# Performance work log

Hardware: AMD Instinct MI355X
Metric: run time of the kernel (lower is better)

The kernel has to match this reference:

```python
import jax, jax.numpy as jnp
import numpy as np

N = 100000      # nodes
E = 3200000     # edges (before self-loops)
IN = 1          # input feature dim
H1, C = 4, 8    # layer1: 4 heads x 8 channels; layer2: 1 head x 8 channels
NEG_SLOPE = 0.2


def setup_inputs() -> dict:
    key = jax.random.key(0)
    ks = jax.random.split(key, 10)
    x = jax.random.normal(ks[0], (N, IN), jnp.float32)
    edge_index = jax.random.randint(ks[1], (2, E), 0, N, dtype=jnp.int32)
    # layer 1 params (GATConv(1, 8, heads=4))
    W1 = jax.random.normal(ks[2], (IN, H1 * C), jnp.float32) * 0.5
    a_src1 = jax.random.normal(ks[3], (H1, C), jnp.float32) * 0.5
    a_dst1 = jax.random.normal(ks[4], (H1, C), jnp.float32) * 0.5
    b1 = jnp.zeros((H1 * C,), jnp.float32)
    # layer 2 params (GATConv(32, 8, heads=1))
    W2 = jax.random.normal(ks[5], (H1 * C, C), jnp.float32) * 0.2
    a_src2 = jax.random.normal(ks[6], (1, C), jnp.float32) * 0.5
    a_dst2 = jax.random.normal(ks[7], (1, C), jnp.float32) * 0.5
    b2 = jnp.zeros((C,), jnp.float32)
    return {"x": x, "edge_index": edge_index, "W1": W1, "a_src1": a_src1,
            "a_dst1": a_dst1, "b1": b1, "W2": W2, "a_src2": a_src2,
            "a_dst2": a_dst2, "b2": b2}


def _gat_layer(x, src, dst, W, a_s, a_d, b, heads, ch):
    # Linear transform per head: [N, heads, ch]
    h = (x @ W).reshape(-1, heads, ch)
    # per-node attention logits
    al_s = jnp.einsum('nhc,hc->nh', h, a_s)  # [N, H]
    al_d = jnp.einsum('nhc,hc->nh', h, a_d)  # [N, H]
    # per-edge logits (message src -> dst)
    e = jax.nn.leaky_relu(al_s[src] + al_d[dst], NEG_SLOPE)  # [E', H]
    # segment softmax over incoming edges of each dst node
    m = jax.ops.segment_max(e, dst, num_segments=N)          # [N, H]
    e = jnp.exp(e - m[dst])
    s = jax.ops.segment_sum(e, dst, num_segments=N)          # [N, H]
    alpha = e / s[dst]                                       # [E', H]
    # weighted scatter-add aggregation
    out = jax.ops.segment_sum(h[src] * alpha[:, :, None], dst, num_segments=N)
    return out.reshape(N, heads * ch) + b


def reference(x, edge_index, W1, a_src1, a_dst1, b1, W2, a_src2, a_dst2, b2):
    loops = jnp.arange(N, dtype=edge_index.dtype)
    src = jnp.concatenate([edge_index[0], loops])  # add self-loops (PyG default)
    dst = jnp.concatenate([edge_index[1], loops])
    h = _gat_layer(x, src, dst, W1, a_src1, a_dst1, b1, H1, C)
    h = jax.nn.relu(h)
    out = _gat_layer(h, src, dst, W2, a_src2, a_dst2, b2, 1, C)
    return out
```

## Files before the change

kernel.cpp:

```cpp
#include <hip/hip_runtime.h>
#include <hip/hip_bf16.h>

#define NEG_SLOPE 0.2f
#define CAPS 8192
#define CAPG 8192
#define CAPA 81920


__global__ void init_cc(int* __restrict__ curA, int* __restrict__ curB,
                        const float* __restrict__ W1,
                        const float* __restrict__ as1,
                        const float* __restrict__ ad1,
                        float* __restrict__ consts) {
    int t = threadIdx.x;
    if (t < 8) {
        int h = t & 3;
        const float* a = (t < 4) ? as1 : ad1;
        float s = 0.f;
        #pragma unroll
        for (int c = 0; c < 8; ++c)
            s += W1[h * 8 + c] * a[h * 8 + c];
        consts[t] = s;
    }
    if (t < 64) curA[t] = t * CAPA;
    curB[t] = t << 13;
}

__global__ void scatterA(const int* __restrict__ ei, int* __restrict__ curA,
                         unsigned int* __restrict__ bufA, int E) {
    __shared__ int cnt[64];
    __shared__ int basel[64];
    int t = threadIdx.x;
    int chunk = (E + gridDim.x - 1) / gridDim.x;
    int lo = blockIdx.x * chunk;
    int hi = min(E, lo + chunk);
    const int* dei = ei + E;
    if (t < 64) cnt[t] = 0;
    __syncthreads();
    bool vec = ((E & 3) == 0);
    int lo4 = (lo + 3) & ~3;
    int end4 = hi & ~3;
    if (vec && end4 > lo4) {
        for (int e = lo + t; e < lo4; e += 1024) atomicAdd(&cnt[dei[e] >> 11], 1);
        const int4* dei4 = (const int4*)dei;
        for (int v = (lo4 >> 2) + t; v < (end4 >> 2); v += 1024) {
            int4 d = dei4[v];
            atomicAdd(&cnt[d.x >> 11], 1); atomicAdd(&cnt[d.y >> 11], 1);
            atomicAdd(&cnt[d.z >> 11], 1); atomicAdd(&cnt[d.w >> 11], 1);
        }
        for (int e = end4 + t; e < hi; e += 1024) atomicAdd(&cnt[dei[e] >> 11], 1);
    } else {
        for (int e = lo + t; e < hi; e += 1024) atomicAdd(&cnt[dei[e] >> 11], 1);
    }
    __syncthreads();
    if (t < 64) {
        int c = cnt[t];
        basel[t] = c ? (atomicAdd(&curA[t], c) - t * CAPA) : 0;
        cnt[t] = 0;
    }
    __syncthreads();
    if (vec && end4 > lo4) {
        for (int e = lo + t; e < lo4; e += 1024) {
            int s = ei[e], d = dei[e]; int sp = d >> 11;
            int off = basel[sp] + atomicAdd(&cnt[sp], 1);
            if (off < CAPA) bufA[sp * CAPA + off] = (unsigned)s | ((unsigned)(d & 2047) << 17);
        }
        const int4* sei4 = (const int4*)ei;
        const int4* dei4 = (const int4*)dei;
        for (int v = (lo4 >> 2) + t; v < (end4 >> 2); v += 1024) {
            int4 sv = sei4[v]; int4 dv = dei4[v];
            int s0 = dv.x >> 11, s1 = dv.y >> 11, s2 = dv.z >> 11, s3 = dv.w >> 11;
            int o0 = basel[s0] + atomicAdd(&cnt[s0], 1);
            if (o0 < CAPA) bufA[s0 * CAPA + o0] = (unsigned)sv.x | ((unsigned)(dv.x & 2047) << 17);
            int o1 = basel[s1] + atomicAdd(&cnt[s1], 1);
            if (o1 < CAPA) bufA[s1 * CAPA + o1] = (unsigned)sv.y | ((unsigned)(dv.y & 2047) << 17);
            int o2 = basel[s2] + atomicAdd(&cnt[s2], 1);
            if (o2 < CAPA) bufA[s2 * CAPA + o2] = (unsigned)sv.z | ((unsigned)(dv.z & 2047) << 17);
            int o3 = basel[s3] + atomicAdd(&cnt[s3], 1);
            if (o3 < CAPA) bufA[s3 * CAPA + o3] = (unsigned)sv.w | ((unsigned)(dv.w & 2047) << 17);
        }
        for (int e = end4 + t; e < hi; e += 1024) {
            int s = ei[e], d = dei[e]; int sp = d >> 11;
            int off = basel[sp] + atomicAdd(&cnt[sp], 1);
            if (off < CAPA) bufA[sp * CAPA + off] = (unsigned)s | ((unsigned)(d & 2047) << 17);
        }
    } else {
        for (int e = lo + t; e < hi; e += 1024) {
            int s = ei[e], d = dei[e]; int sp = d >> 11;
            int off = basel[sp] + atomicAdd(&cnt[sp], 1);
            if (off < CAPA) bufA[sp * CAPA + off] = (unsigned)s | ((unsigned)(d & 2047) << 17);
        }
    }
}

__global__ void scatterB(const int* __restrict__ curA, int* __restrict__ curB,
                         const unsigned int* __restrict__ bufA,
                         unsigned int* __restrict__ pairs) {
    __shared__ int cnt[16];
    __shared__ int basel[16];
    int t = threadIdx.x;
    int sp = blockIdx.x >> 3;
    int part = blockIdx.x & 7;
    int base = sp * CAPA;
    int fill = min(curA[sp] - base, CAPA);
    if (fill <= 0) return;
    int lo = (fill * part) >> 3;
    int hi = (fill * (part + 1)) >> 3;
    for (int c0 = lo; c0 < hi; c0 += 8192) {
        int cend = min(hi, c0 + 8192);
        if (t < 16) cnt[t] = 0;
        __syncthreads();
        for (int i = c0 + t; i < cend; i += 1024)
            atomicAdd(&cnt[(bufA[base + i] >> 24) & 15], 1);
        __syncthreads();
        if (t < 16) {
            int c = cnt[t];
            int bkg = (sp << 4) + t;
            basel[t] = c ? (atomicAdd(&curB[bkg], c) - (bkg << 13)) : 0;
            cnt[t] = 0;
        }
        __syncthreads();
        for (int i = c0 + t; i < cend; i += 1024) {
            unsigned p = bufA[base + i];
            int b16 = (p >> 24) & 15;
            int off = basel[b16] + atomicAdd(&cnt[b16], 1);
            if (off < CAPG) pairs[(((sp << 4) + b16) << 13) + off] = p & 0x00FFFFFFu;
        }
        __syncthreads();
    }
}

__global__ __launch_bounds__(512, 8)
void l1_comb(const float* __restrict__ x,
             const int* __restrict__ curB,
             const unsigned int* __restrict__ pairs,
             unsigned int* __restrict__ gsorted, int* __restrict__ bmeta,
             const float* __restrict__ consts,
             const float* __restrict__ W1, const float* __restrict__ b1,
             const float* __restrict__ W2,
             const float* __restrict__ as2, const float* __restrict__ ad2,
             float* __restrict__ h2, float* __restrict__ als2,
             float* __restrict__ ald2, int N) {
    __shared__ unsigned sbuf[CAPS];
    __shared__ int hcnt[128], offs[128], hcur[128];
    __shared__ float xl[128];
    int t = threadIdx.x;
    int bk = blockIdx.x;
    int node0 = bk << 7;
    int nw = min(128, N - node0);
    if (t < 128) xl[t] = (t < nw) ? x[node0 + t] : 0.f;
    float S[4], D[4];
    #pragma unroll
    for (int h = 0; h < 4; ++h) { S[h] = consts[h]; D[h] = consts[4 + h]; }
    int base = bk << 13;
    int clen = min(curB[bk] - base, CAPG);
    int clen6 = min(clen, 6144);
    int g = t >> 2, jj = t & 3;
    unsigned pr[12];
    const uint4* pairs4 = (const uint4*)(pairs + base);
    #pragma unroll
    for (int k = 0; k < 3; ++k) {
        int w4 = t + (k << 9);
        int wi = w4 << 2;
        if (wi + 3 < clen6) {
            uint4 v = pairs4[w4];
            pr[4 * k]     = v.x; pr[4 * k + 1] = v.y;
            pr[4 * k + 2] = v.z; pr[4 * k + 3] = v.w;
        } else {
            #pragma unroll
            for (int m = 0; m < 4; ++m)
                pr[4 * k + m] = (wi + m < clen6) ? pairs[base + wi + m] : 0xFFFFFFFFu;
        }
    }
    if (t < 128) hcnt[t] = 0;
    __syncthreads();
    #pragma unroll
    for (int k = 0; k < 12; ++k)
        if (pr[k] != 0xFFFFFFFFu) atomicAdd(&hcnt[pr[k] >> 17], 1);
    for (int idx = 6144 + t; idx < clen; idx += 512)
        atomicAdd(&hcnt[pairs[base + idx] >> 17], 1);
    __syncthreads();
    if (t < 64) {
        int h0 = hcnt[2 * t], h1 = hcnt[2 * t + 1];
        int s = h0 + h1, sc_ = s;
        #pragma unroll
        for (int o = 1; o < 64; o <<= 1) {
            int u = __shfl_up(sc_, o);
            if (t >= o) sc_ += u;
        }
        int excl = sc_ - s;
        offs[2 * t] = excl;          hcur[2 * t] = excl;
        offs[2 * t + 1] = excl + h0; hcur[2 * t + 1] = excl + h0;
    }
    __syncthreads();
    #pragma unroll
    for (int k = 0; k < 12; ++k)
        if (pr[k] != 0xFFFFFFFFu) {
            int loc = atomicAdd(&hcur[pr[k] >> 17], 1);
            sbuf[loc] = pr[k];
        }
    for (int idx = 6144 + t; idx < clen; idx += 512) {
        unsigned p = pairs[base + idx];
        int loc = atomicAdd(&hcur[p >> 17], 1);
        sbuf[loc] = p;
    }
    __syncthreads();
    {
        int clen4 = clen & ~3;
        for (int i = t << 2; i < clen4; i += 2048) {
            uint4 v = *(const uint4*)&sbuf[i];
            *(uint4*)&gsorted[base + i] = v;
        }
        for (int i = clen4 + t; i < clen; i += 512) gsorted[base + i] = sbuf[i];
    }
    if (t < 128) bmeta[(bk << 7) + t] = offs[t] | (hcnt[t] << 14);
    float xd = xl[g];
    float sacc[4] = {0.f, 0.f, 0.f, 0.f};
    float tacc[4] = {0.f, 0.f, 0.f, 0.f};
    int st = offs[g], en = st + hcnt[g];
    int i = st + jj;
    while (i + 28 < en) {
        unsigned p0 = sbuf[i],      p1 = sbuf[i + 4],  p2 = sbuf[i + 8],
                 p3 = sbuf[i + 12], p4 = sbuf[i + 16], p5 = sbuf[i + 20],
                 p6 = sbuf[i + 24], p7 = sbuf[i + 28];
        float x0 = x[p0 & 131071u], x1 = x[p1 & 131071u];
        float x2 = x[p2 & 131071u], x3 = x[p3 & 131071u];
        float x4 = x[p4 & 131071u], x5 = x[p5 & 131071u];
        float x6 = x[p6 & 131071u], x7 = x[p7 & 131071u];
        float xs_[8] = {x0, x1, x2, x3, x4, x5, x6, x7};
        #pragma unroll
        for (int q = 0; q < 8; ++q) {
            float xs = xs_[q];
            #pragma unroll
            for (int h = 0; h < 4; ++h) {
                float v = xs * S[h] + xd * D[h];
                v = (v > 0.f) ? v : NEG_SLOPE * v;
                float w = __expf(v);
                sacc[h] += w;
                tacc[h] = fmaf(w, xs, tacc[h]);
            }
        }
        i += 32;
    }
    for (; i < en; i += 4) {
        float xs = x[sbuf[i] & 131071u];
        #pragma unroll
        for (int h = 0; h < 4; ++h) {
            float v = xs * S[h] + xd * D[h];
            v = (v > 0.f) ? v : NEG_SLOPE * v;
            float w = __expf(v);
            sacc[h] += w;
            tacc[h] = fmaf(w, xs, tacc[h]);
        }
    }
    #pragma unroll
    for (int h = 0; h < 4; ++h) {
        sacc[h] += __shfl_xor(sacc[h], 1); sacc[h] += __shfl_xor(sacc[h], 2);
        tacc[h] += __shfl_xor(tacc[h], 1); tacc[h] += __shfl_xor(tacc[h], 2);
    }
    if (jj == 0 && g < nw) {
        int n = node0 + g;
        float xn = xd;
        float o[8];
        #pragma unroll
        for (int c = 0; c < 8; ++c) o[c] = 0.f;
        #pragma unroll
        for (int h = 0; h < 4; ++h) {
            float v = xn * (S[h] + D[h]);
            v = (v > 0.f) ? v : NEG_SLOPE * v;
            float ww = __expf(v);
            float s1 = ww + sacc[h];
            float t1 = ww * xn + tacc[h];
            float tt = t1 / s1;
            #pragma unroll
            for (int c = 0; c < 8; ++c) {
                float rr = fmaxf(tt * W1[h * 8 + c] + b1[h * 8 + c], 0.f);
                #pragma unroll
                for (int c2 = 0; c2 < 8; ++c2) o[c2] += rr * W2[(h * 8 + c) * 8 + c2];
            }
        }
        float as = 0.f, ad = 0.f;
        #pragma unroll
        for (int c = 0; c < 8; ++c) { as += o[c] * as2[c]; ad += o[c] * ad2[c]; }
        float4* hv = (float4*)&h2[(size_t)n * 8];
        hv[0] = make_float4(o[0], o[1], o[2], o[3]);
        hv[1] = make_float4(o[4], o[5], o[6], o[7]);
        als2[n] = as;
        ald2[n] = ad;
    }
}

__global__ __launch_bounds__(512, 8)
void l2_comb(const int* __restrict__ curB,
             const unsigned int* __restrict__ gsorted,
             const int* __restrict__ bmeta,
             const float* __restrict__ als2, const float* __restrict__ ald2,
             const float* __restrict__ h2, const float* __restrict__ b2,
             float* __restrict__ out, int N) {
    __shared__ unsigned runl[CAPS];
    __shared__ float adl[128];
    int t = threadIdx.x;
    int bk = blockIdx.x;
    int node0 = bk << 7;
    int nw = min(128, N - node0);
    if (t < 128) adl[t] = (t < nw) ? ald2[node0 + t] : 0.f;
    int base = bk << 13;
    int clen = min(curB[bk] - base, CAPG);
    {
        int clen4 = clen & ~3;
        const uint4* g4 = (const uint4*)(gsorted + base);
        for (int i = t << 2; i < clen4; i += 2048) {
            uint4 v = g4[i >> 2];
            *(uint4*)&runl[i] = v;
        }
        for (int i = clen4 + t; i < clen; i += 512) runl[i] = gsorted[base + i];
    }
    __syncthreads();
    int g = t >> 2, j = t & 3;
    int jh = j & 1;
    int jp = j >> 1;
    if (g >= nw) return;
    int pk = bmeta[(bk << 7) + g];
    int st = pk & 16383, cgn = pk >> 14;
    const unsigned* run = runl + st;
    float adv = adl[g];
    int co = jh << 2;
    float4 acc = make_float4(0.f, 0.f, 0.f, 0.f);
    float sw = 0.f;
    int k = 0;
    while (2 * k + 8 <= cgn) {
        unsigned q0 = run[2 * k + jp];
        unsigned q1 = run[2 * k + 2 + jp];
        unsigned q2 = run[2 * k + 4 + jp];
        unsigned q3 = run[2 * k + 6 + jp];
        size_t r0 = (size_t)(q0 & 131071u) * 8 + co;
        size_t r1 = (size_t)(q1 & 131071u) * 8 + co;
        size_t r2 = (size_t)(q2 & 131071u) * 8 + co;
        size_t r3 = (size_t)(q3 & 131071u) * 8 + co;
        float4 h0 = *(const float4*)&h2[r0];
        float4 h1 = *(const float4*)&h2[r1];
        float4 h2v = *(const float4*)&h2[r2];
        float4 h3 = *(const float4*)&h2[r3];
        float a0 = als2[q0 & 131071u], a1 = als2[q1 & 131071u];
        float a2 = als2[q2 & 131071u], a3 = als2[q3 & 131071u];
        float aa[4] = {a0, a1, a2, a3};
        float4 hh[4] = {h0, h1, h2v, h3};
        #pragma unroll
        for (int q = 0; q < 4; ++q) {
            float v = aa[q] + adv;
            v = (v > 0.f) ? v : NEG_SLOPE * v;
            float w = __expf(v);
            sw += w;
            acc.x = fmaf(w, hh[q].x, acc.x);
            acc.y = fmaf(w, hh[q].y, acc.y);
            acc.z = fmaf(w, hh[q].z, acc.z);
            acc.w = fmaf(w, hh[q].w, acc.w);
        }
        k += 4;
    }
    for (; 2 * k + jp < cgn; ++k) {
        unsigned q = run[2 * k + jp];
        size_t r = (size_t)(q & 131071u) * 8 + co;
        float4 hq = *(const float4*)&h2[r];
        float a = als2[q & 131071u];
        float v = a + adv;
        v = (v > 0.f) ? v : NEG_SLOPE * v;
        float w = __expf(v);
        sw += w;
        acc.x = fmaf(w, hq.x, acc.x);
        acc.y = fmaf(w, hq.y, acc.y);
        acc.z = fmaf(w, hq.z, acc.z);
        acc.w = fmaf(w, hq.w, acc.w);
    }
    acc.x += __shfl_xor(acc.x, 2); acc.y += __shfl_xor(acc.y, 2);
    acc.z += __shfl_xor(acc.z, 2); acc.w += __shfl_xor(acc.w, 2);
    sw += __shfl_xor(sw, 2);
    int n = node0 + g;
    float v = als2[n] + adv;
    v = (v > 0.f) ? v : NEG_SLOPE * v;
    float ww = __expf(v);
    float4 hs = *(const float4*)&h2[(size_t)n * 8 + co];
    float inv = 1.f / (sw + ww);
    if (jp == 0) {
        float4 bb = *(const float4*)&b2[co];
        *(float4*)&out[(size_t)n * 8 + co] = make_float4(
            (acc.x + ww * hs.x) * inv + bb.x,
            (acc.y + ww * hs.y) * inv + bb.y,
            (acc.z + ww * hs.z) * inv + bb.z,
            (acc.w + ww * hs.w) * inv + bb.w);
    }
}


__global__ void prep_consts(const float* __restrict__ W1,
                            const float* __restrict__ as1,
                            const float* __restrict__ ad1,
                            float* __restrict__ consts) {
    int t = threadIdx.x;
    if (t >= 8) return;
    int h = t & 3;
    const float* a = (t < 4) ? as1 : ad1;
    float s = 0.f;
    #pragma unroll
    for (int c = 0; c < 8; ++c)
        s += W1[h * 8 + c] * a[h * 8 + c];
    consts[t] = s;
}

__global__ void edge_pass1(const int* __restrict__ ei, const float* __restrict__ x,
                           const float* __restrict__ consts,
                           float* __restrict__ s1, float* __restrict__ t1, int E, int N) {
    int e = blockIdx.x * blockDim.x + threadIdx.x;
    if (e >= E + N) return;
    int src, dst;
    if (e < E) { src = ei[e]; dst = ei[E + e]; }
    else       { src = dst = e - E; }
    float xs = x[src], xd = x[dst];
    #pragma unroll
    for (int h = 0; h < 4; ++h) {
        float v = xs * consts[h] + xd * consts[4 + h];
        v = (v > 0.f) ? v : NEG_SLOPE * v;
        float w = __expf(v);
        atomicAdd(&s1[dst * 4 + h], w);
        atomicAdd(&t1[dst * 4 + h], w * xs);
    }
}

__global__ void node_mid(const float* __restrict__ s1, const float* __restrict__ t1,
                         const float* __restrict__ W1, const float* __restrict__ b1,
                         const float* __restrict__ W2,
                         const float* __restrict__ as2, const float* __restrict__ ad2,
                         float* __restrict__ h2, float* __restrict__ als2,
                         float* __restrict__ ald2, int N) {
    int n = blockIdx.x * blockDim.x + threadIdx.x;
    if (n >= N) return;
    float o[8];
    #pragma unroll
    for (int c = 0; c < 8; ++c) o[c] = 0.f;
    #pragma unroll
    for (int h = 0; h < 4; ++h) {
        float t = t1[n * 4 + h] / s1[n * 4 + h];
        #pragma unroll
        for (int c = 0; c < 8; ++c) {
            float r = fmaxf(t * W1[h * 8 + c] + b1[h * 8 + c], 0.f);
            #pragma unroll
            for (int c2 = 0; c2 < 8; ++c2) o[c2] += r * W2[(h * 8 + c) * 8 + c2];
        }
    }
    float as = 0.f, ad = 0.f;
    #pragma unroll
    for (int c = 0; c < 8; ++c) { h2[n * 8 + c] = o[c]; as += o[c] * as2[c]; ad += o[c] * ad2[c]; }
    als2[n] = as; ald2[n] = ad;
}

__global__ void edge_pass2(const int* __restrict__ ei, const float* __restrict__ als2,
                           const float* __restrict__ ald2, const float* __restrict__ h2,
                           float* __restrict__ s2, float* __restrict__ acc2, int E, int N) {
    int e = blockIdx.x * blockDim.x + threadIdx.x;
    if (e >= E + N) return;
    int src, dst;
    if (e < E) { src = ei[e]; dst = ei[E + e]; }
    else       { src = dst = e - E; }
    float v = als2[src] + ald2[dst];
    v = (v > 0.f) ? v : NEG_SLOPE * v;
    float w = __expf(v);
    atomicAdd(&s2[dst], w);
    const float4* hs = (const float4*)&h2[src * 8];
    float4 a = hs[0], bq = hs[1];
    float* acc = &acc2[dst * 8];
    atomicAdd(&acc[0], w * a.x);  atomicAdd(&acc[1], w * a.y);
    atomicAdd(&acc[2], w * a.z);  atomicAdd(&acc[3], w * a.w);
    atomicAdd(&acc[4], w * bq.x); atomicAdd(&acc[5], w * bq.y);
    atomicAdd(&acc[6], w * bq.z); atomicAdd(&acc[7], w * bq.w);
}

__global__ void node_out(const float* __restrict__ s2, const float* __restrict__ acc2,
                         const float* __restrict__ b2, float* __restrict__ out, int N) {
    int i = blockIdx.x * blockDim.x + threadIdx.x;
    if (i >= N * 8) return;
    out[i] = acc2[i] / s2[i >> 3] + b2[i & 7];
}


extern "C" void kernel_launch(void* const* d_in, const int* in_sizes, int n_in,
                              void* d_out, int out_size, void* d_ws, size_t ws_size,
                              hipStream_t stream) {
    const float* x   = (const float*)d_in[0];
    const int*   ei  = (const int*)d_in[1];
    const float* W1  = (const float*)d_in[2];
    const float* as1 = (const float*)d_in[3];
    const float* ad1 = (const float*)d_in[4];
    const float* b1  = (const float*)d_in[5];
    const float* W2  = (const float*)d_in[6];
    const float* as2 = (const float*)d_in[7];
    const float* ad2 = (const float*)d_in[8];
    const float* b2  = (const float*)d_in[9];
    float* out = (float*)d_out;

    const int N = in_sizes[0];
    const int E = in_sizes[1] / 2;
    const int NBK = (N + 127) >> 7;

    float* ws = (float*)d_ws;
    size_t need = ((size_t)16 + 64 + 1024 + 131072 + 10 * (size_t)N
                   + 2 * (size_t)1024 * CAPG + (size_t)64 * CAPA) * sizeof(float);

    if (N <= 131072 && ws_size >= need) {
        float*    consts  = ws;
        int*      curA    = (int*)(ws + 16);
        int*      curB    = curA + 64;
        int*      bmeta   = curB + 1024;
        float*    als2    = (float*)(bmeta + 131072);
        float*    ald2    = als2 + N;
        float*    h2      = ald2 + N;
        unsigned* pairs   = (unsigned*)(h2 + 8 * (size_t)N);
        unsigned* gsorted = pairs + (size_t)1024 * CAPG;
        unsigned* bufA    = gsorted + (size_t)1024 * CAPG;

        init_cc<<<1, 1024, 0, stream>>>(curA, curB, W1, as1, ad1, consts);
        scatterA<<<256, 1024, 0, stream>>>(ei, curA, bufA, E);
        scatterB<<<512, 1024, 0, stream>>>(curA, curB, bufA, pairs);
        l1_comb<<<NBK, 512, 0, stream>>>(x, curB, pairs, gsorted, bmeta, consts,
                                         W1, b1, W2, as2, ad2, h2, als2, ald2, N);
        l2_comb<<<NBK, 512, 0, stream>>>(curB, gsorted, bmeta, als2, ald2, h2, b2, out, N);
    } else {
        float* consts = ws;
        float* s1   = ws + 16;
        float* t1   = s1 + 4 * (size_t)N;
        float* h2   = t1 + 4 * (size_t)N;
        float* als2 = h2 + 8 * (size_t)N;
        float* ald2 = als2 + (size_t)N;
        float* s2   = ald2 + (size_t)N;
        float* acc2 = s2 + (size_t)N;

        hipMemsetAsync(ws, 0, (16 + 8 * (size_t)N) * sizeof(float), stream);
        hipMemsetAsync(s2, 0, 9 * (size_t)N * sizeof(float), stream);
        prep_consts<<<1, 64, 0, stream>>>(W1, as1, ad1, consts);
        int total = E + N;
        edge_pass1<<<(total + 255) / 256, 256, 0, stream>>>(ei, x, consts, s1, t1, E, N);
        node_mid<<<(N + 255) / 256, 256, 0, stream>>>(s1, t1, W1, b1, W2, as2, ad2, h2, als2, ald2, N);
        edge_pass2<<<(total + 255) / 256, 256, 0, stream>>>(ei, als2, ald2, h2, s2, acc2, E, N);
        node_out<<<(N * 8 + 255) / 256, 256, 0, stream>>>(s2, acc2, b2, out, N);
    }
}
```

Baseline: 179.2 us.

## Use per-block fixed segments in scatterA to drop count pass and global atomics

scatterA now writes each block's edges for a superbucket into a fixed-width private segment, and records the per-block fill in a table. This removes the separate counting pass over the destination indices and the global atomic reservation on curA. scatterB reads its 32 segments using the fill table. The init kernel is replaced by a memset, and the per-head attention constants are recomputed inside l1_comb. The risk is that a segment overflows (fixed cap of 384 entries per block per superbucket) and silently drops edges when the degree distribution is skewed; scatterB also makes a second pass over bufA with per-segment loops.

```diff
diff --git a/kernel.cpp b/kernel.cpp
--- a/kernel.cpp
+++ b/kernel.cpp
@@ -4,35 +4,18 @@
 #define NEG_SLOPE 0.2f
 #define CAPS 8192
 #define CAPG 8192
-#define CAPA 81920
-
-
-__global__ void init_cc(int* __restrict__ curA, int* __restrict__ curB,
-                        const float* __restrict__ W1,
-                        const float* __restrict__ as1,
-                        const float* __restrict__ ad1,
-                        float* __restrict__ consts) {
+#define SEGW 384
+#define CAPA (256 * SEGW)
+
+
+__global__ void scatterA(const int* __restrict__ ei,
+                         unsigned int* __restrict__ bufA,
+                         int* __restrict__ fillT, int E) {
+    __shared__ int cnt[64];
     int t = threadIdx.x;
-    if (t < 8) {
-        int h = t & 3;
-        const float* a = (t < 4) ? as1 : ad1;
-        float s = 0.f;
-        #pragma unroll
-        for (int c = 0; c < 8; ++c)
-            s += W1[h * 8 + c] * a[h * 8 + c];
-        consts[t] = s;
-    }
-    if (t < 64) curA[t] = t * CAPA;
-    curB[t] = t << 13;
-}
-
-__global__ void scatterA(const int* __restrict__ ei, int* __restrict__ curA,
-                         unsigned int* __restrict__ bufA, int E) {
-    __shared__ int cnt[64];
-    __shared__ int basel[64];
-    int t = threadIdx.x;
+    int blk = blockIdx.x;
     int chunk = (E + gridDim.x - 1) / gridDim.x;
-    int lo = blockIdx.x * chunk;
+    int lo = blk * chunk;
     int hi = min(E, lo + chunk);
     const int* dei = ei + E;
     if (t < 64) cnt[t] = 0;
@@ -41,59 +24,42 @@
     int lo4 = (lo + 3) & ~3;
     int end4 = hi & ~3;
     if (vec && end4 > lo4) {
-        for (int e = lo + t; e < lo4; e += 1024) atomicAdd(&cnt[dei[e] >> 11], 1);
-        const int4* dei4 = (const int4*)dei;
-        for (int v = (lo4 >> 2) + t; v < (end4 >> 2); v += 1024) {
-            int4 d = dei4[v];
-            atomicAdd(&cnt[d.x >> 11], 1); atomicAdd(&cnt[d.y >> 11], 1);
-            atomicAdd(&cnt[d.z >> 11], 1); atomicAdd(&cnt[d.w >> 11], 1);
-        }
-        for (int e = end4 + t; e < hi; e += 1024) atomicAdd(&cnt[dei[e] >> 11], 1);
-    } else {
-        for (int e = lo + t; e < hi; e += 1024) atomicAdd(&cnt[dei[e] >> 11], 1);
-    }
-    __syncthreads();
-    if (t < 64) {
-        int c = cnt[t];
-        basel[t] = c ? (atomicAdd(&curA[t], c) - t * CAPA) : 0;
-        cnt[t] = 0;
-    }
-    __syncthreads();
-    if (vec && end4 > lo4) {
         for (int e = lo + t; e < lo4; e += 1024) {
             int s = ei[e], d = dei[e]; int sp = d >> 11;
-            int off = basel[sp] + atomicAdd(&cnt[sp], 1);
-            if (off < CAPA) bufA[sp * CAPA + off] = (unsigned)s | ((unsigned)(d & 2047) << 17);
+            int off = atomicAdd(&cnt[sp], 1);
+            if (off < SEGW) bufA[sp * CAPA + blk * SEGW + off] = (unsigned)s | ((unsigned)(d & 2047) << 17);
         }
         const int4* sei4 = (const int4*)ei;
         const int4* dei4 = (const int4*)dei;
         for (int v = (lo4 >> 2) + t; v < (end4 >> 2); v += 1024) {
             int4 sv = sei4[v]; int4 dv = dei4[v];
             int s0 = dv.x >> 11, s1 = dv.y >> 11, s2 = dv.z >> 11, s3 = dv.w >> 11;
-            int o0 = basel[s0] + atomicAdd(&cnt[s0], 1);
-            if (o0 < CAPA) bufA[s0 * CAPA + o0] = (unsigned)sv.x | ((unsigned)(dv.x & 2047) << 17);
-            int o1 = basel[s1] + atomicAdd(&cnt[s1], 1);
-            if (o1 < CAPA) bufA[s1 * CAPA + o1] = (unsigned)sv.y | ((unsigned)(dv.y & 2047) << 17);
-            int o2 = basel[s2] + atomicAdd(&cnt[s2], 1);
-            if (o2 < CAPA) bufA[s2 * CAPA + o2] = (unsigned)sv.z | ((unsigned)(dv.z & 2047) << 17);
-            int o3 = basel[s3] + atomicAdd(&cnt[s3], 1);
-            if (o3 < CAPA) bufA[s3 * CAPA + o3] = (unsigned)sv.w | ((unsigned)(dv.w & 2047) << 17);
+            int o0 = atomicAdd(&cnt[s0], 1);
+            if (o0 < SEGW) bufA[s0 * CAPA + blk * SEGW + o0] = (unsigned)sv.x | ((unsigned)(dv.x & 2047) << 17);
+            int o1 = atomicAdd(&cnt[s1], 1);
+            if (o1 < SEGW) bufA[s1 * CAPA + blk * SEGW + o1] = (unsigned)sv.y | ((unsigned)(dv.y & 2047) << 17);
+            int o2 = atomicAdd(&cnt[s2], 1);
+            if (o2 < SEGW) bufA[s2 * CAPA + blk * SEGW + o2] = (unsigned)sv.z | ((unsigned)(dv.z & 2047) << 17);
+            int o3 = atomicAdd(&cnt[s3], 1);
+            if (o3 < SEGW) bufA[s3 * CAPA + blk * SEGW + o3] = (unsigned)sv.w | ((unsigned)(dv.w & 2047) << 17);
         }
         for (int e = end4 + t; e < hi; e += 1024) {
             int s = ei[e], d = dei[e]; int sp = d >> 11;
-            int off = basel[sp] + atomicAdd(&cnt[sp], 1);
-            if (off < CAPA) bufA[sp * CAPA + off] = (unsigned)s | ((unsigned)(d & 2047) << 17);
+            int off = atomicAdd(&cnt[sp], 1);
+            if (off < SEGW) bufA[sp * CAPA + blk * SEGW + off] = (unsigned)s | ((unsigned)(d & 2047) << 17);
         }
     } else {
         for (int e = lo + t; e < hi; e += 1024) {
             int s = ei[e], d = dei[e]; int sp = d >> 11;
-            int off = basel[sp] + atomicAdd(&cnt[sp], 1);
-            if (off < CAPA) bufA[sp * CAPA + off] = (unsigned)s | ((unsigned)(d & 2047) << 17);
-        }
-    }
-}
-
-__global__ void scatterB(const int* __restrict__ curA, int* __restrict__ curB,
+            int off = atomicAdd(&cnt[sp], 1);
+            if (off < SEGW) bufA[sp * CAPA + blk * SEGW + off] = (unsigned)s | ((unsigned)(d & 2047) << 17);
+        }
+    }
+    __syncthreads();
+    if (t < 64) fillT[blk * 64 + t] = min(cnt[t], SEGW);
+}
+
+__global__ void scatterB(const int* __restrict__ fillT, int* __restrict__ curB,
                          const unsigned int* __restrict__ bufA,
                          unsigned int* __restrict__ pairs) {
     __shared__ int cnt[16];
@@ -101,32 +67,31 @@
     int t = threadIdx.x;
     int sp = blockIdx.x >> 3;
     int part = blockIdx.x & 7;
-    int base = sp * CAPA;
-    int fill = min(curA[sp] - base, CAPA);
-    if (fill <= 0) return;
-    int lo = (fill * part) >> 3;
-    int hi = (fill * (part + 1)) >> 3;
-    for (int c0 = lo; c0 < hi; c0 += 8192) {
-        int cend = min(hi, c0 + 8192);
-        if (t < 16) cnt[t] = 0;
-        __syncthreads();
-        for (int i = c0 + t; i < cend; i += 1024)
-            atomicAdd(&cnt[(bufA[base + i] >> 24) & 15], 1);
-        __syncthreads();
-        if (t < 16) {
-            int c = cnt[t];
-            int bkg = (sp << 4) + t;
-            basel[t] = c ? (atomicAdd(&curB[bkg], c) - (bkg << 13)) : 0;
-            cnt[t] = 0;
-        }
-        __syncthreads();
-        for (int i = c0 + t; i < cend; i += 1024) {
-            unsigned p = bufA[base + i];
+    int seg0 = part * 32, seg1 = seg0 + 32;
+    if (t < 16) cnt[t] = 0;
+    __syncthreads();
+    for (int seg = seg0; seg < seg1; ++seg) {
+        int len = fillT[seg * 64 + sp];
+        const unsigned* src = bufA + sp * CAPA + seg * SEGW;
+        for (int i = t; i < len; i += 1024)
+            atomicAdd(&cnt[(src[i] >> 24) & 15], 1);
+    }
+    __syncthreads();
+    if (t < 16) {
+        int c = cnt[t];
+        basel[t] = c ? atomicAdd(&curB[(sp << 4) + t], c) : 0;
+        cnt[t] = 0;
+    }
+    __syncthreads();
+    for (int seg = seg0; seg < seg1; ++seg) {
+        int len = fillT[seg * 64 + sp];
+        const unsigned* src = bufA + sp * CAPA + seg * SEGW;
+        for (int i = t; i < len; i += 1024) {
+            unsigned p = src[i];
             int b16 = (p >> 24) & 15;
             int off = basel[b16] + atomicAdd(&cnt[b16], 1);
             if (off < CAPG) pairs[(((sp << 4) + b16) << 13) + off] = p & 0x00FFFFFFu;
         }
-        __syncthreads();
     }
 }
 
@@ -135,8 +100,8 @@
              const int* __restrict__ curB,
              const unsigned int* __restrict__ pairs,
              unsigned int* __restrict__ gsorted, int* __restrict__ bmeta,
-             const float* __restrict__ consts,
-             const float* __restrict__ W1, const float* __restrict__ b1,
+             const float* __restrict__ W1, const float* __restrict__ as1,
+             const float* __restrict__ ad1, const float* __restrict__ b1,
              const float* __restrict__ W2,
              const float* __restrict__ as2, const float* __restrict__ ad2,
              float* __restrict__ h2, float* __restrict__ als2,
@@ -151,9 +116,18 @@
     if (t < 128) xl[t] = (t < nw) ? x[node0 + t] : 0.f;
     float S[4], D[4];
     #pragma unroll
-    for (int h = 0; h < 4; ++h) { S[h] = consts[h]; D[h] = consts[4 + h]; }
+    for (int h = 0; h < 4; ++h) {
+        float s = 0.f, dv = 0.f;
+        #pragma unroll
+        for (int c = 0; c < 8; ++c) {
+            float w = W1[h * 8 + c];
+            s += w * as1[h * 8 + c];
+            dv += w * ad1[h * 8 + c];
+        }
+        S[h] = s; D[h] = dv;
+    }
     int base = bk << 13;
-    int clen = min(curB[bk] - base, CAPG);
+    int clen = min(curB[bk], CAPG);
     int clen6 = min(clen, 6144);
     int g = t >> 2, jj = t & 3;
     unsigned pr[12];
@@ -305,7 +279,7 @@
     int nw = min(128, N - node0);
     if (t < 128) adl[t] = (t < nw) ? ald2[node0 + t] : 0.f;
     int base = bk << 13;
-    int clen = min(curB[bk] - base, CAPG);
+    int clen = min(curB[bk], CAPG);
     {
         int clen4 = clen & ~3;
         const uint4* g4 = (const uint4*)(gsorted + base);
@@ -502,14 +476,13 @@
     const int NBK = (N + 127) >> 7;
 
     float* ws = (float*)d_ws;
-    size_t need = ((size_t)16 + 64 + 1024 + 131072 + 10 * (size_t)N
+    size_t need = ((size_t)1024 + 16384 + 131072 + 10 * (size_t)N
                    + 2 * (size_t)1024 * CAPG + (size_t)64 * CAPA) * sizeof(float);
 
     if (N <= 131072 && ws_size >= need) {
-        float*    consts  = ws;
-        int*      curA    = (int*)(ws + 16);
-        int*      curB    = curA + 64;
-        int*      bmeta   = curB + 1024;
+        int*      curB    = (int*)ws;
+        int*      fillT   = curB + 1024;
+        int*      bmeta   = fillT + 16384;
         float*    als2    = (float*)(bmeta + 131072);
         float*    ald2    = als2 + N;
         float*    h2      = ald2 + N;
@@ -517,11 +490,12 @@
         unsigned* gsorted = pairs + (size_t)1024 * CAPG;
         unsigned* bufA    = gsorted + (size_t)1024 * CAPG;
 
-        init_cc<<<1, 1024, 0, stream>>>(curA, curB, W1, as1, ad1, consts);
-        scatterA<<<256, 1024, 0, stream>>>(ei, curA, bufA, E);
-        scatterB<<<512, 1024, 0, stream>>>(curA, curB, bufA, pairs);
-        l1_comb<<<NBK, 512, 0, stream>>>(x, curB, pairs, gsorted, bmeta, consts,
-                                         W1, b1, W2, as2, ad2, h2, als2, ald2, N);
+        hipMemsetAsync(curB, 0, 1024 * sizeof(int), stream);
+        scatterA<<<256, 1024, 0, stream>>>(ei, bufA, fillT, E);
+        scatterB<<<512, 1024, 0, stream>>>(fillT, curB, bufA, pairs);
+        l1_comb<<<NBK, 512, 0, stream>>>(x, curB, pairs, gsorted, bmeta,
+                                         W1, as1, ad1, b1, W2, as2, ad2,
+                                         h2, als2, ald2, N);
         l2_comb<<<NBK, 512, 0, stream>>>(curB, gsorted, bmeta, als2, ald2, h2, b2, out, N);
     } else {
         float* consts = ws;
```

After: 203.2 us. 1.13x slower.
